# Kernel tuning notes

Measured on AMD Instinct MI355X. Metric: run time of the kernel, lower is better.

The kernel has to match this reference:

```python
import jax, jax.numpy as jnp
import numpy as np

N_NODES = 100000
NEG_SLOPE = 0.01  # F.leaky_relu default


def _gin_mean_layer(x, src, dst):
    """DGL GINConv(aggregator='mean', apply_func=None, eps=0, activation=leaky_relu).
    out = leaky_relu((1+eps)*x + mean_{in-neighbors} x_src), nodes with no in-edges get mean=0.
    """
    msg_sum = jax.ops.segment_sum(x[src], dst, num_segments=N_NODES)  # [N, D]
    deg = jax.ops.segment_sum(jnp.ones(src.shape, dtype=x.dtype), dst, num_segments=N_NODES)  # [N]
    mean = msg_sum / jnp.maximum(deg, 1.0)[:, None]
    return jax.nn.leaky_relu(x + mean, negative_slope=NEG_SLOPE)


def setup_inputs() -> dict:
    key = jax.random.key(0)
    k0, k1, k2, k3, k4 = jax.random.split(key, 5)
    n_edges = 640000
    d = 128
    return {
        "node_features": jax.random.normal(k0, (N_NODES, d), dtype=jnp.float32),
        "edges1_src": jax.random.randint(k1, (n_edges,), 0, N_NODES, dtype=jnp.int64),
        "edges1_dst": jax.random.randint(k2, (n_edges,), 0, N_NODES, dtype=jnp.int64),
        "edges2_src": jax.random.randint(k3, (n_edges,), 0, N_NODES, dtype=jnp.int64),
        "edges2_dst": jax.random.randint(k4, (n_edges,), 0, N_NODES, dtype=jnp.int64),
    }


def reference(node_features, edges1_src, edges1_dst, edges2_src, edges2_dst):
    h_AC1 = _gin_mean_layer(node_features, edges1_src, edges1_dst)
    h_CA1 = _gin_mean_layer(node_features, edges2_src, edges2_dst)
    h = jnp.concatenate((h_AC1, h_CA1), axis=1)  # [N, 2D]
    h_AC2 = _gin_mean_layer(h, edges1_src, edges1_dst)
    h_CA2 = _gin_mean_layer(h, edges2_src, edges2_dst)
    return jnp.concatenate((h_AC2, h_CA2), axis=1)  # [N, 4D]
```

## Files before the change

### kernel.cpp

```cpp
#include <hip/hip_runtime.h>

#define N_NODES 100000
#define NEG 0.01f
#define CAP 32
#define EDGE_ILP 8

typedef float f4v __attribute__((ext_vector_type(4)));

__device__ __forceinline__ float lrelu(float v) { return v > 0.f ? v : NEG * v; }

__device__ __forceinline__ unsigned int f2bf(float f) {
    unsigned int x = __float_as_uint(f);
    return (x + 0x7fffu + ((x >> 16) & 1u)) >> 16;
}
__device__ __forceinline__ unsigned int pack2bf(float lo, float hi) {
    return f2bf(lo) | (f2bf(hi) << 16);
}
__device__ __forceinline__ float bf_lo(unsigned int u) { return __uint_as_float(u << 16); }
__device__ __forceinline__ float bf_hi(unsigned int u) { return __uint_as_float(u & 0xffff0000u); }

__device__ __forceinline__ void unpack8(uint4 u, float* f) {
    f[0] = bf_lo(u.x); f[1] = bf_hi(u.x);
    f[2] = bf_lo(u.y); f[3] = bf_hi(u.y);
    f[4] = bf_lo(u.z); f[5] = bf_hi(u.z);
    f[6] = bf_lo(u.w); f[7] = bf_hi(u.w);
}

__device__ __forceinline__ unsigned int packq(float v, int sh) {
    float c = fminf(fmaxf(v * 16.f, -127.f), 127.f);
    int q = __float2int_rn(c);
    return ((unsigned int)(q & 255)) << sh;
}
__device__ __forceinline__ uint2 pack8i8(const float* f) {
    uint2 r;
    r.x = packq(f[0], 0) | packq(f[1], 8) | packq(f[2], 16) | packq(f[3], 24);
    r.y = packq(f[4], 0) | packq(f[5], 8) | packq(f[6], 16) | packq(f[7], 24);
    return r;
}
__device__ __forceinline__ void addsext8(uint2 u, int* acc) {
    acc[0] += ((int)(u.x << 24)) >> 24;
    acc[1] += ((int)(u.x << 16)) >> 24;
    acc[2] += ((int)(u.x <<  8)) >> 24;
    acc[3] += ((int)u.x) >> 24;
    acc[4] += ((int)(u.y << 24)) >> 24;
    acc[5] += ((int)(u.y << 16)) >> 24;
    acc[6] += ((int)(u.y <<  8)) >> 24;
    acc[7] += ((int)u.y) >> 24;
}

__global__ void __launch_bounds__(256) build_and_convert(
        const int* __restrict__ s1, const int* __restrict__ d1a, int E1,
        const int* __restrict__ s2, const int* __restrict__ d2a, int E2,
        int* __restrict__ deg1, int* __restrict__ slots1,
        int* __restrict__ deg2, int* __restrict__ slots2,
        const float4* __restrict__ x, uint4* __restrict__ xb,
        int edgeBlocks, int edgeThreads) {
    int b = blockIdx.x;
    if (b < edgeBlocks) {
        int tid = b * 256 + threadIdx.x;
        int E = E1 + E2;
        #pragma unroll
        for (int k = 0; k < EDGE_ILP; ++k) {
            int e = tid + k * edgeThreads;
            if (e < E1) {
                int d = d1a[e];
                int pos = atomicAdd(&deg1[d], 1);
                if (pos < CAP) slots1[d * CAP + pos] = s1[e];
            } else if (e < E) {
                int q = e - E1;
                int d = d2a[q];
                int pos = atomicAdd(&deg2[d], 1);
                if (pos < CAP) slots2[d * CAP + pos] = s2[q];
            }
        }
    } else {
        int i = (b - edgeBlocks) * 256 + threadIdx.x;
        if (i >= N_NODES * 16) return;
        float4 v0 = x[2 * i];
        float4 v1 = x[2 * i + 1];
        uint4 p;
        p.x = pack2bf(v0.x, v0.y);
        p.y = pack2bf(v0.z, v0.w);
        p.z = pack2bf(v1.x, v1.y);
        p.w = pack2bf(v1.z, v1.w);
        xb[i] = p;
    }
}

__global__ void __launch_bounds__(256) layer1(
        const uint4* __restrict__ x4,
        const int* __restrict__ deg1, const int* __restrict__ slots1,
        const int* __restrict__ deg2, const int* __restrict__ slots2,
        uint4* __restrict__ h4, uint2* __restrict__ hi8) {
    int gid = blockIdx.x * blockDim.x + threadIdx.x;
    int n = gid >> 6;
    if (n >= N_NODES) return;
    int lane = gid & 63;
    int t = lane & 15;
    int g = lane >> 4;
    int lane31 = lane & 31;

    int d1 = deg1[n], d2 = deg2[n];
    int v1 = slots1[n * CAP + lane31];
    int v2 = slots2[n * CAP + lane31];
    uint4 xv = x4[(size_t)n * 16 + t];

    int m1 = min(d1, CAP), m2 = min(d2, CAP);

    int sel = (lane < 32) ? v1 : v2;
    int m_own = (g < 2) ? m1 : m2;
    int base = (g < 2) ? 0 : 32;
    int sub = g & 1;
    int L = max((m1 + 1) >> 1, (m2 + 1) >> 1);

    float acc[8] = {0.f, 0.f, 0.f, 0.f, 0.f, 0.f, 0.f, 0.f};

    int jj0 = sub, jj1 = sub + 2;
    int s0 = __shfl(sel, base + jj0);
    int s1 = __shfl(sel, base + jj1);
    uint4 u0 = make_uint4(0u, 0u, 0u, 0u);
    uint4 u1 = make_uint4(0u, 0u, 0u, 0u);
    if (jj0 < m_own) u0 = x4[(size_t)s0 * 16 + t];
    if (jj1 < m_own) u1 = x4[(size_t)s1 * 16 + t];
    for (int i = 0; i < L; ++i) {
        uint4 cur = u0; u0 = u1;
        int jn = 2 * (i + 2) + sub;
        int sn = __shfl(sel, (base + jn) & 63);
        u1 = make_uint4(0u, 0u, 0u, 0u);
        if (jn < m_own) u1 = x4[(size_t)sn * 16 + t];
        float f[8]; unpack8(cur, f);
        #pragma unroll
        for (int i8 = 0; i8 < 8; ++i8) acc[i8] += f[i8];
    }

    #pragma unroll
    for (int i8 = 0; i8 < 8; ++i8) acc[i8] += __shfl_xor(acc[i8], 16);

    float xf[8]; unpack8(xv, xf);
    float r = (g < 2) ? 1.f / (float)max(d1, 1) : 1.f / (float)max(d2, 1);

    float o[8];
    #pragma unroll
    for (int i8 = 0; i8 < 8; ++i8) o[i8] = lrelu(xf[i8] + acc[i8] * r);

    if (g == 0) {
        uint4 ob;
        ob.x = pack2bf(o[0], o[1]); ob.y = pack2bf(o[2], o[3]);
        ob.z = pack2bf(o[4], o[5]); ob.w = pack2bf(o[6], o[7]);
        h4[(size_t)n * 32 + t] = ob;
    } else if (g == 2) {
        uint4 ob;
        ob.x = pack2bf(o[0], o[1]); ob.y = pack2bf(o[2], o[3]);
        ob.z = pack2bf(o[4], o[5]); ob.w = pack2bf(o[6], o[7]);
        h4[(size_t)n * 32 + 16 + t] = ob;
    } else if (g == 1) {
        hi8[(size_t)n * 32 + t] = pack8i8(o);
    } else {
        hi8[(size_t)n * 32 + 16 + t] = pack8i8(o);
    }
}

__global__ void __launch_bounds__(256) layer2(
        const uint4* __restrict__ h4, const uint2* __restrict__ hi8,
        const int* __restrict__ deg1, const int* __restrict__ slots1,
        const int* __restrict__ deg2, const int* __restrict__ slots2,
        float4* __restrict__ out4) {
    int gid = blockIdx.x * blockDim.x + threadIdx.x;
    int n = gid >> 6;
    if (n >= N_NODES) return;
    int lane = gid & 63;
    int t = lane & 31;
    int g = lane >> 5;
    int lane31 = lane & 31;

    int d1 = deg1[n], d2 = deg2[n];
    int v1 = slots1[n * CAP + lane31];
    int v2 = slots2[n * CAP + lane31];
    uint4 hv = h4[(size_t)n * 32 + t];

    int m1 = min(d1, CAP), m2 = min(d2, CAP);

    int sel = (lane < 32) ? v1 : v2;
    int m_own = (g == 0) ? m1 : m2;
    int base = g << 5;
    int L = max(m1, m2);

    int acc[8] = {0, 0, 0, 0, 0, 0, 0, 0};

    int s0 = __shfl(sel, base);
    int s1 = __shfl(sel, base + 1);
    uint2 u0 = make_uint2(0u, 0u);
    uint2 u1 = make_uint2(0u, 0u);
    if (0 < m_own) u0 = hi8[(size_t)s0 * 32 + t];
    if (1 < m_own) u1 = hi8[(size_t)s1 * 32 + t];
    for (int i = 0; i < L; ++i) {
        uint2 cur = u0; u0 = u1;
        int jn = i + 2;
        int sn = __shfl(sel, (base + jn) & 63);
        u1 = make_uint2(0u, 0u);
        if (jn < m_own) u1 = hi8[(size_t)sn * 32 + t];
        addsext8(cur, acc);
    }

    float hf[8]; unpack8(hv, hf);
    float r = (g == 0) ? 1.f / (float)max(d1, 1) : 1.f / (float)max(d2, 1);
    float s = r * 0.0625f;

    f4v* ob = (f4v*)out4;
    f4v O0 = {lrelu(hf[0] + (float)acc[0] * s), lrelu(hf[1] + (float)acc[1] * s),
              lrelu(hf[2] + (float)acc[2] * s), lrelu(hf[3] + (float)acc[3] * s)};
    f4v O1 = {lrelu(hf[4] + (float)acc[4] * s), lrelu(hf[5] + (float)acc[5] * s),
              lrelu(hf[6] + (float)acc[6] * s), lrelu(hf[7] + (float)acc[7] * s)};
    size_t off = (size_t)n * 128 + (size_t)g * 64 + 2 * t;
    __builtin_nontemporal_store(O0, &ob[off]);
    __builtin_nontemporal_store(O1, &ob[off + 1]);
}

extern "C" void kernel_launch(void* const* d_in, const int* in_sizes, int n_in,
                              void* d_out, int out_size, void* d_ws, size_t ws_size,
                              hipStream_t stream) {
    const float* x = (const float*)d_in[0];
    const int* e1s = (const int*)d_in[1];
    const int* e1d = (const int*)d_in[2];
    const int* e2s = (const int*)d_in[3];
    const int* e2d = (const int*)d_in[4];
    const int E1 = in_sizes[1];
    const int E2 = in_sizes[3];
    float* out = (float*)d_out;

    int* deg1   = (int*)d_ws;
    int* deg2   = deg1 + N_NODES;
    int* slots1 = deg2 + N_NODES;
    int* slots2 = slots1 + (size_t)N_NODES * CAP;
    unsigned int* xb = (unsigned int*)(slots2 + (size_t)N_NODES * CAP);
    unsigned int* hb = xb + (size_t)N_NODES * 64;
    uint2* hi8 = (uint2*)(hb + (size_t)N_NODES * 128);

    hipMemsetAsync(deg1, 0, 2ull * N_NODES * sizeof(int), stream);

    int convBlocks = (N_NODES * 16 + 255) / 256;
    int edgeThreads = ((E1 + E2 + EDGE_ILP - 1) / EDGE_ILP + 255) / 256 * 256;
    int edgeBlocks = edgeThreads / 256;
    build_and_convert<<<edgeBlocks + convBlocks, 256, 0, stream>>>(
        e1s, e1d, E1, e2s, e2d, E2, deg1, slots1, deg2, slots2,
        (const float4*)x, (uint4*)xb, edgeBlocks, edgeThreads);

    int blocks = (N_NODES + 3) / 4;
    layer1<<<blocks, 256, 0, stream>>>(
        (const uint4*)xb, deg1, slots1, deg2, slots2, (uint4*)hb, hi8);
    layer2<<<blocks, 256, 0, stream>>>(
        (const uint4*)hb, hi8, deg1, slots1, deg2, slots2, (float4*)out);
}
```

Measured before the change: 449.1 us.

## Gather int8 node features in layer1 and widen per-lane gather loads to 16 bytes

The convert pass now also writes an int8-quantized copy of the input features. Layer1 gathers neighbour rows from this int8 copy instead of the bf16 one, which halves the gather bytes, and sums them in integer accumulators. Both layers now load 16 bytes per lane (16 int8 values), so more edges are processed in parallel per wave, with cross-group shuffle reductions afterwards. EDGE_ILP is raised to 16. The cost is extra quantization error in layer1, more registers per lane, and some lanes sitting idle during stores.

Measured after the change: 578.7 us. +28.8%, slower.

```diff
diff --git a/kernel.cpp b/kernel.cpp
--- a/kernel.cpp
+++ b/kernel.cpp
@@ -3,7 +3,7 @@
 #define N_NODES 100000
 #define NEG 0.01f
 #define CAP 32
-#define EDGE_ILP 8
+#define EDGE_ILP 16
 
 typedef float f4v __attribute__((ext_vector_type(4)));
 
@@ -47,6 +47,10 @@
     acc[6] += ((int)(u.y <<  8)) >> 24;
     acc[7] += ((int)u.y) >> 24;
 }
+__device__ __forceinline__ void addsext16(uint4 u, int* acc) {
+    addsext8(make_uint2(u.x, u.y), acc);
+    addsext8(make_uint2(u.z, u.w), acc + 8);
+}
 
 __global__ void __launch_bounds__(256) build_and_convert(
         const int* __restrict__ s1, const int* __restrict__ d1a, int E1,
@@ -54,7 +58,7 @@
         int* __restrict__ deg1, int* __restrict__ slots1,
         int* __restrict__ deg2, int* __restrict__ slots2,
         const float4* __restrict__ x, uint4* __restrict__ xb,
-        int edgeBlocks, int edgeThreads) {
+        uint2* __restrict__ xi8, int edgeBlocks, int edgeThreads) {
     int b = blockIdx.x;
     if (b < edgeBlocks) {
         int tid = b * 256 + threadIdx.x;
@@ -84,84 +88,93 @@
         p.z = pack2bf(v1.x, v1.y);
         p.w = pack2bf(v1.z, v1.w);
         xb[i] = p;
+        float f[8] = {v0.x, v0.y, v0.z, v0.w, v1.x, v1.y, v1.z, v1.w};
+        xi8[i] = pack8i8(f);
     }
 }
 
 __global__ void __launch_bounds__(256) layer1(
-        const uint4* __restrict__ x4,
+        const uint4* __restrict__ x4, const uint4* __restrict__ xi8_4,
         const int* __restrict__ deg1, const int* __restrict__ slots1,
         const int* __restrict__ deg2, const int* __restrict__ slots2,
-        uint4* __restrict__ h4, uint2* __restrict__ hi8) {
+        uint4* __restrict__ h4, uint4* __restrict__ hi8_4) {
     int gid = blockIdx.x * blockDim.x + threadIdx.x;
     int n = gid >> 6;
     if (n >= N_NODES) return;
     int lane = gid & 63;
-    int t = lane & 15;
-    int g = lane >> 4;
+    int tl = lane & 7;
+    int g = lane >> 3;
     int lane31 = lane & 31;
 
     int d1 = deg1[n], d2 = deg2[n];
     int v1 = slots1[n * CAP + lane31];
     int v2 = slots2[n * CAP + lane31];
-    uint4 xv = x4[(size_t)n * 16 + t];
+    uint4 xv0 = x4[(size_t)n * 16 + 2 * tl];
+    uint4 xv1 = x4[(size_t)n * 16 + 2 * tl + 1];
 
     int m1 = min(d1, CAP), m2 = min(d2, CAP);
 
     int sel = (lane < 32) ? v1 : v2;
-    int m_own = (g < 2) ? m1 : m2;
-    int base = (g < 2) ? 0 : 32;
-    int sub = g & 1;
-    int L = max((m1 + 1) >> 1, (m2 + 1) >> 1);
-
-    float acc[8] = {0.f, 0.f, 0.f, 0.f, 0.f, 0.f, 0.f, 0.f};
-
-    int jj0 = sub, jj1 = sub + 2;
+    int m_own = (g < 4) ? m1 : m2;
+    int base = (g < 4) ? 0 : 32;
+    int sub = g & 3;
+    int L = max((m1 + 3) >> 2, (m2 + 3) >> 2);
+
+    int acc[16];
+    #pragma unroll
+    for (int i = 0; i < 16; ++i) acc[i] = 0;
+
+    int jj0 = sub, jj1 = sub + 4;
     int s0 = __shfl(sel, base + jj0);
-    int s1 = __shfl(sel, base + jj1);
+    int s1v = __shfl(sel, base + jj1);
     uint4 u0 = make_uint4(0u, 0u, 0u, 0u);
     uint4 u1 = make_uint4(0u, 0u, 0u, 0u);
-    if (jj0 < m_own) u0 = x4[(size_t)s0 * 16 + t];
-    if (jj1 < m_own) u1 = x4[(size_t)s1 * 16 + t];
+    if (jj0 < m_own) u0 = xi8_4[(size_t)s0 * 8 + tl];
+    if (jj1 < m_own) u1 = xi8_4[(size_t)s1v * 8 + tl];
     for (int i = 0; i < L; ++i) {
         uint4 cur = u0; u0 = u1;
-        int jn = 2 * (i + 2) + sub;
+        int jn = 4 * (i + 2) + sub;
         int sn = __shfl(sel, (base + jn) & 63);
         u1 = make_uint4(0u, 0u, 0u, 0u);
-        if (jn < m_own) u1 = x4[(size_t)sn * 16 + t];
-        float f[8]; unpack8(cur, f);
-        #pragma unroll
-        for (int i8 = 0; i8 < 8; ++i8) acc[i8] += f[i8];
-    }
-
-    #pragma unroll
-    for (int i8 = 0; i8 < 8; ++i8) acc[i8] += __shfl_xor(acc[i8], 16);
-
-    float xf[8]; unpack8(xv, xf);
-    float r = (g < 2) ? 1.f / (float)max(d1, 1) : 1.f / (float)max(d2, 1);
-
-    float o[8];
-    #pragma unroll
-    for (int i8 = 0; i8 < 8; ++i8) o[i8] = lrelu(xf[i8] + acc[i8] * r);
-
-    if (g == 0) {
-        uint4 ob;
-        ob.x = pack2bf(o[0], o[1]); ob.y = pack2bf(o[2], o[3]);
-        ob.z = pack2bf(o[4], o[5]); ob.w = pack2bf(o[6], o[7]);
-        h4[(size_t)n * 32 + t] = ob;
-    } else if (g == 2) {
-        uint4 ob;
-        ob.x = pack2bf(o[0], o[1]); ob.y = pack2bf(o[2], o[3]);
-        ob.z = pack2bf(o[4], o[5]); ob.w = pack2bf(o[6], o[7]);
-        h4[(size_t)n * 32 + 16 + t] = ob;
-    } else if (g == 1) {
-        hi8[(size_t)n * 32 + t] = pack8i8(o);
-    } else {
-        hi8[(size_t)n * 32 + 16 + t] = pack8i8(o);
+        if (jn < m_own) u1 = xi8_4[(size_t)sn * 8 + tl];
+        addsext16(cur, acc);
+    }
+
+    #pragma unroll
+    for (int i = 0; i < 16; ++i) {
+        acc[i] += __shfl_xor(acc[i], 8);
+        acc[i] += __shfl_xor(acc[i], 16);
+    }
+
+    float xf[16];
+    unpack8(xv0, xf);
+    unpack8(xv1, xf + 8);
+    float r = (g < 4) ? 1.f / (float)max(d1, 1) : 1.f / (float)max(d2, 1);
+    float s = r * 0.0625f;
+
+    float o[16];
+    #pragma unroll
+    for (int i = 0; i < 16; ++i) o[i] = lrelu(xf[i] + (float)acc[i] * s);
+
+    if (g == 0 || g == 4) {
+        uint4 a, b;
+        a.x = pack2bf(o[0], o[1]);  a.y = pack2bf(o[2], o[3]);
+        a.z = pack2bf(o[4], o[5]);  a.w = pack2bf(o[6], o[7]);
+        b.x = pack2bf(o[8], o[9]);  b.y = pack2bf(o[10], o[11]);
+        b.z = pack2bf(o[12], o[13]); b.w = pack2bf(o[14], o[15]);
+        size_t off = (size_t)n * 32 + ((g == 4) ? 16 : 0) + 2 * tl;
+        h4[off] = a;
+        h4[off + 1] = b;
+    } else if (g == 1 || g == 5) {
+        uint2 lo = pack8i8(o);
+        uint2 hi = pack8i8(o + 8);
+        uint4 q = make_uint4(lo.x, lo.y, hi.x, hi.y);
+        hi8_4[(size_t)n * 16 + ((g == 5) ? 8 : 0) + tl] = q;
     }
 }
 
 __global__ void __launch_bounds__(256) layer2(
-        const uint4* __restrict__ h4, const uint2* __restrict__ hi8,
+        const uint4* __restrict__ h4, const uint4* __restrict__ hi8_4,
         const int* __restrict__ deg1, const int* __restrict__ slots1,
         const int* __restrict__ deg2, const int* __restrict__ slots2,
         float4* __restrict__ out4) {
@@ -169,51 +182,65 @@
     int n = gid >> 6;
     if (n >= N_NODES) return;
     int lane = gid & 63;
-    int t = lane & 31;
-    int g = lane >> 5;
+    int tl = lane & 15;
+    int g = lane >> 4;
     int lane31 = lane & 31;
 
     int d1 = deg1[n], d2 = deg2[n];
     int v1 = slots1[n * CAP + lane31];
     int v2 = slots2[n * CAP + lane31];
-    uint4 hv = h4[(size_t)n * 32 + t];
+    uint4 hv0 = h4[(size_t)n * 32 + 2 * tl];
+    uint4 hv1 = h4[(size_t)n * 32 + 2 * tl + 1];
 
     int m1 = min(d1, CAP), m2 = min(d2, CAP);
 
     int sel = (lane < 32) ? v1 : v2;
-    int m_own = (g == 0) ? m1 : m2;
-    int base = g << 5;
-    int L = max(m1, m2);
-
-    int acc[8] = {0, 0, 0, 0, 0, 0, 0, 0};
-
-    int s0 = __shfl(sel, base);
-    int s1 = __shfl(sel, base + 1);
-    uint2 u0 = make_uint2(0u, 0u);
-    uint2 u1 = make_uint2(0u, 0u);
-    if (0 < m_own) u0 = hi8[(size_t)s0 * 32 + t];
-    if (1 < m_own) u1 = hi8[(size_t)s1 * 32 + t];
+    int m_own = (g < 2) ? m1 : m2;
+    int base = (g < 2) ? 0 : 32;
+    int sub = g & 1;
+    int L = max((m1 + 1) >> 1, (m2 + 1) >> 1);
+
+    int acc[16];
+    #pragma unroll
+    for (int i = 0; i < 16; ++i) acc[i] = 0;
+
+    int jj0 = sub, jj1 = sub + 2;
+    int s0 = __shfl(sel, base + jj0);
+    int s1v = __shfl(sel, base + jj1);
+    uint4 u0 = make_uint4(0u, 0u, 0u, 0u);
+    uint4 u1 = make_uint4(0u, 0u, 0u, 0u);
+    if (jj0 < m_own) u0 = hi8_4[(size_t)s0 * 16 + tl];
+    if (jj1 < m_own) u1 = hi8_4[(size_t)s1v * 16 + tl];
     for (int i = 0; i < L; ++i) {
-        uint2 cur = u0; u0 = u1;
-        int jn = i + 2;
+        uint4 cur = u0; u0 = u1;
+        int jn = 2 * (i + 2) + sub;
         int sn = __shfl(sel, (base + jn) & 63);
-        u1 = make_uint2(0u, 0u);
-        if (jn < m_own) u1 = hi8[(size_t)sn * 32 + t];
-        addsext8(cur, acc);
-    }
-
-    float hf[8]; unpack8(hv, hf);
-    float r = (g == 0) ? 1.f / (float)max(d1, 1) : 1.f / (float)max(d2, 1);
+        u1 = make_uint4(0u, 0u, 0u, 0u);
+        if (jn < m_own) u1 = hi8_4[(size_t)sn * 16 + tl];
+        addsext16(cur, acc);
+    }
+
+    #pragma unroll
+    for (int i = 0; i < 16; ++i) acc[i] += __shfl_xor(acc[i], 16);
+
+    float hf[16];
+    unpack8(hv0, hf);
+    unpack8(hv1, hf + 8);
+    float r = (g < 2) ? 1.f / (float)max(d1, 1) : 1.f / (float)max(d2, 1);
     float s = r * 0.0625f;
 
-    f4v* ob = (f4v*)out4;
-    f4v O0 = {lrelu(hf[0] + (float)acc[0] * s), lrelu(hf[1] + (float)acc[1] * s),
-              lrelu(hf[2] + (float)acc[2] * s), lrelu(hf[3] + (float)acc[3] * s)};
-    f4v O1 = {lrelu(hf[4] + (float)acc[4] * s), lrelu(hf[5] + (float)acc[5] * s),
-              lrelu(hf[6] + (float)acc[6] * s), lrelu(hf[7] + (float)acc[7] * s)};
-    size_t off = (size_t)n * 128 + (size_t)g * 64 + 2 * t;
-    __builtin_nontemporal_store(O0, &ob[off]);
-    __builtin_nontemporal_store(O1, &ob[off + 1]);
+    if (g == 0 || g == 2) {
+        f4v* ob = (f4v*)out4;
+        size_t off = (size_t)n * 128 + ((g == 2) ? 64 : 0) + 4 * tl;
+        #pragma unroll
+        for (int q = 0; q < 4; ++q) {
+            f4v O = {lrelu(hf[4 * q + 0] + (float)acc[4 * q + 0] * s),
+                     lrelu(hf[4 * q + 1] + (float)acc[4 * q + 1] * s),
+                     lrelu(hf[4 * q + 2] + (float)acc[4 * q + 2] * s),
+                     lrelu(hf[4 * q + 3] + (float)acc[4 * q + 3] * s)};
+            __builtin_nontemporal_store(O, &ob[off + q]);
+        }
+    }
 }
 
 extern "C" void kernel_launch(void* const* d_in, const int* in_sizes, int n_in,
@@ -234,7 +261,8 @@
     int* slots2 = slots1 + (size_t)N_NODES * CAP;
     unsigned int* xb = (unsigned int*)(slots2 + (size_t)N_NODES * CAP);
     unsigned int* hb = xb + (size_t)N_NODES * 64;
-    uint2* hi8 = (uint2*)(hb + (size_t)N_NODES * 128);
+    unsigned int* hi8 = hb + (size_t)N_NODES * 128;
+    unsigned int* xi8 = hi8 + (size_t)N_NODES * 64;
 
     hipMemsetAsync(deg1, 0, 2ull * N_NODES * sizeof(int), stream);
 
@@ -243,11 +271,13 @@
     int edgeBlocks = edgeThreads / 256;
     build_and_convert<<<edgeBlocks + convBlocks, 256, 0, stream>>>(
         e1s, e1d, E1, e2s, e2d, E2, deg1, slots1, deg2, slots2,
-        (const float4*)x, (uint4*)xb, edgeBlocks, edgeThreads);
+        (const float4*)x, (uint4*)xb, (uint2*)xi8, edgeBlocks, edgeThreads);
 
     int blocks = (N_NODES + 3) / 4;
     layer1<<<blocks, 256, 0, stream>>>(
-        (const uint4*)xb, deg1, slots1, deg2, slots2, (uint4*)hb, hi8);
+        (const uint4*)xb, (const uint4*)xi8, deg1, slots1, deg2, slots2,
+        (uint4*)hb, (uint4*)hi8);
     layer2<<<blocks, 256, 0, stream>>>(
-        (const uint4*)hb, hi8, deg1, slots1, deg2, slots2, (float4*)out);
-}
+        (const uint4*)hb, (const uint4*)hi8, deg1, slots1, deg2, slots2,
+        (float4*)out);
+}
```
